# Kernel tuning notes

Measured on AMD Instinct MI355X. Metric: run time of the kernel, lower is better.

## Reference

```python
import jax, jax.numpy as jnp
import numpy as np

N = 50000      # nodes
E = 1600000    # message edges (avg degree 32)
EQ = 500000    # link-prediction query edges
IN, HID, OUT, FCH = 128, 128, 64, 256
ALPHA = 0.5


def setup_inputs() -> dict:
    key = jax.random.key(0)
    ks = jax.random.split(key, 8)
    def p(k, shape):
        fan_in = shape[0]
        return jax.random.normal(k, shape, jnp.float32) * (1.0 / np.sqrt(fan_in))
    return {
        "x": jax.random.normal(ks[0], (N, IN), jnp.float32),
        "edge_index": jax.random.randint(ks[1], (2, E), 0, N),
        "edge_label_index": jax.random.randint(ks[2], (2, EQ), 0, N),
        "W1": p(ks[3], (IN, HID)),  "b1": jnp.zeros((HID,), jnp.float32),
        "W2": p(ks[4], (HID, OUT)), "b2": jnp.zeros((OUT,), jnp.float32),
        "Wf1": p(ks[5], (IN, FCH)), "bf1": jnp.zeros((FCH,), jnp.float32),
        "Wf2": p(ks[6], (FCH, OUT)), "bf2": jnp.zeros((OUT,), jnp.float32),
    }


def reference(x, edge_index, edge_label_index, W1, b1, W2, b2, Wf1, bf1, Wf2, bf2):
    n = x.shape[0]
    # GCN self-loops + symmetric normalization (PyG GCNConv defaults)
    loop = jnp.arange(n)
    src = jnp.concatenate([edge_index[0], loop])
    dst = jnp.concatenate([edge_index[1], loop])
    deg = jax.ops.segment_sum(jnp.ones_like(dst, jnp.float32), dst, num_segments=n)
    dinv = jnp.where(deg > 0, jax.lax.rsqrt(deg), 0.0)
    norm = dinv[src] * dinv[dst]  # [E+N]

    def gcn(h, W, b):
        h = h @ W                                  # transform first (PyG order)
        msg = norm[:, None] * h[src]               # gather + scale per edge
        return jax.ops.segment_sum(msg, dst, num_segments=n) + b

    x_gcn = jax.nn.relu(gcn(x, W1, b1))
    x_gcn = gcn(x_gcn, W2, b2)
    x_fc = jax.nn.relu(x @ Wf1 + bf1) @ Wf2 + bf2
    z = x_gcn * (1.0 - ALPHA) + x_fc * ALPHA       # [N, OUT]
    # edge dot-product decode
    return jnp.sum(z[edge_label_index[0]] * z[edge_label_index[1]], axis=1)
```

## Files before the change

### kernel.cpp

```cpp
#include <hip/hip_runtime.h>

#define FIN   128
#define FHID  128
#define FOUT  64
#define FFC   256
#define CHUNK 8192
#define BKBITS 7
#define BKN   128
#define ECAP  4608

typedef __attribute__((ext_vector_type(8))) short          bf16x8;
typedef __attribute__((ext_vector_type(4))) float          f32x4;
typedef __attribute__((ext_vector_type(2))) float          f32x2;
typedef __attribute__((ext_vector_type(8))) unsigned short u16x8;

static __device__ __forceinline__ unsigned short f2bf(float f) {
    unsigned int u = __float_as_uint(f);
    u = (u + 0x7fffu + ((u >> 16) & 1u)) >> 16;
    return (unsigned short)u;
}
static __device__ __forceinline__ float bf2f(unsigned short s) {
    return __uint_as_float(((unsigned int)s) << 16);
}

__global__ __launch_bounds__(256) void cvt_binA_kernel(
    const float* __restrict__ x, const float* __restrict__ W1,
    const float* __restrict__ W2, const float* __restrict__ Wf1,
    const float* __restrict__ Wf2,
    unsigned short* __restrict__ xbf, unsigned short* __restrict__ w1t,
    unsigned short* __restrict__ w2t, unsigned short* __restrict__ wf1t,
    unsigned short* __restrict__ wf2t, long n4,
    const int* __restrict__ src, const int* __restrict__ dst,
    int* __restrict__ bcur, unsigned int* __restrict__ ebuf, int E, int NBA)
{
    int t = threadIdx.x;
    if (blockIdx.x < NBA) {
        __shared__ int hist[512];
        __shared__ int rstart[512];
        __shared__ int lcur[512];
        hist[t] = 0; hist[t + 256] = 0; lcur[t] = 0; lcur[t + 256] = 0;
        __syncthreads();
        int e0 = blockIdx.x * CHUNK;
        int e1 = min(e0 + CHUNK, E);
        for (int e = e0 + t; e < e1; e += 256)
            atomicAdd(&hist[dst[e] >> BKBITS], 1);
        __syncthreads();
        if (hist[t])       rstart[t]       = atomicAdd(&bcur[t],       hist[t]);
        if (hist[t + 256]) rstart[t + 256] = atomicAdd(&bcur[t + 256], hist[t + 256]);
        __syncthreads();
        for (int e = e0 + t; e < e1; e += 256) {
            int s = src[e], d = dst[e];
            int b = d >> BKBITS;
            int pos = rstart[b] + atomicAdd(&lcur[b], 1);
            if (pos < ECAP)
                ebuf[(size_t)b * ECAP + pos] =
                    ((unsigned)s << BKBITS) | ((unsigned)d & (BKN - 1));
        }
        return;
    }
    long i = (long)(blockIdx.x - NBA) * 256 + t;
    if (i < 16384) {
        int k = (int)i >> 7, n = (int)i & 127;
        w1t[n * 128 + k] = f2bf(W1[i]);
    } else if (i < 24576) {
        int j = (int)i - 16384; int k = j >> 6, n = j & 63;
        w2t[n * 128 + k] = f2bf(W2[j]);
    } else if (i < 57344) {
        int j = (int)i - 24576; int k = j >> 8, n = j & 255;
        wf1t[n * 128 + k] = f2bf(Wf1[j]);
    } else if (i < 73728) {
        int j = (int)i - 57344; int k = j >> 6, n = j & 63;
        wf2t[n * 256 + k] = f2bf(Wf2[j]);
    } else {
        long xt = i - 73728;
        long g = xt >> 8;
        int  tt = (int)(xt & 255);
        long b0 = g * 1024 + tt;
        #pragma unroll
        for (int k = 0; k < 4; k++) {
            long idx = b0 + (long)k * 256;
            if (idx < n4) {
                float4 v = ((const float4*)x)[idx];
                ushort4 o = make_ushort4(f2bf(v.x), f2bf(v.y), f2bf(v.z), f2bf(v.w));
                ((ushort4*)xbf)[idx] = o;
            }
        }
    }
}

__global__ __launch_bounds__(256) void binB_kernel(
    const unsigned int* __restrict__ ebuf, const int* __restrict__ bcnt,
    int2* __restrict__ rp2, int* __restrict__ col, float* __restrict__ dinv,
    const unsigned short* __restrict__ xbf, unsigned char* __restrict__ xs,
    int N)
{
    __shared__ int cnt[128];
    __shared__ int tmp[256];
    __shared__ int ccur[128];
    __shared__ int scur[256];
    __shared__ float sdinv[128];
    __shared__ unsigned int skey[ECAP];
    int b = blockIdx.x;
    int t = threadIdx.x;
    size_t base = (size_t)b * ECAP;
    int ne = min(bcnt[b], ECAP);
    if (t < 128) cnt[t] = 0;
    scur[t] = 0;
    __syncthreads();
    for (int e = t; e < ne; e += 256) {
        unsigned int k = ebuf[base + e];
        atomicAdd(&cnt[k & (BKN - 1)], 1);
        atomicAdd(&scur[k >> 15], 1);
    }
    __syncthreads();
    int c = (t < 128) ? cnt[t] : 0;
    tmp[t] = c;
    __syncthreads();
    int acc = c;
    for (int off = 1; off < 128; off <<= 1) {
        int a = (t >= off) ? tmp[t - off] : 0;
        __syncthreads();
        acc += a; tmp[t] = acc;
        __syncthreads();
    }
    if (t < 128) {
        float di = rsqrtf((float)c + 1.0f);
        sdinv[t] = di;
        int node = b * BKN + t;
        int st = (int)base + acc - c;
        if (node < N) { dinv[node] = di; rp2[node] = make_int2(st, st + c); }
        ccur[t] = st;
    }
    __syncthreads();
    int sv = scur[t];
    tmp[t] = sv;
    __syncthreads();
    int sacc = sv;
    for (int off = 1; off < 256; off <<= 1) {
        int a = (t >= off) ? tmp[t - off] : 0;
        __syncthreads();
        sacc += a; tmp[t] = sacc;
        __syncthreads();
    }
    scur[t] = sacc - sv;
    __syncthreads();
    for (int e = t; e < ne; e += 256) {
        unsigned int k = ebuf[base + e];
        int pos = atomicAdd(&scur[k >> 15], 1);
        skey[pos] = k;
    }
    __syncthreads();
    for (int w = 0; w < ne; w += 256) {
        int e = w + t;
        if (e < ne) {
            unsigned int k = skey[e];
            int pos = atomicAdd(&ccur[k & (BKN - 1)], 1);
            col[pos] = (int)(k >> BKBITS);
        }
        __syncthreads();
    }
    int nl0 = t >> 3;
    int f0 = (t & 7) << 4;
    #pragma unroll
    for (int it = 0; it < 4; it++) {
        int nl = it * 32 + nl0;
        int gn = b * BKN + nl;
        if (gn >= N) continue;
        float d2 = sdinv[nl];
        const unsigned short* xr = xbf + (size_t)gn * FIN + f0;
        u16x8 v0 = *(const u16x8*)xr;
        u16x8 v1 = *(const u16x8*)(xr + 8);
        float f[16];
        #pragma unroll
        for (int j = 0; j < 8; j++) {
            f[j]     = d2 * bf2f((unsigned short)v0[j]);
            f[8 + j] = d2 * bf2f((unsigned short)v1[j]);
        }
        uint4 w;
        w.x = 0; w.y = 0; w.z = 0; w.w = 0;
        w.x = __builtin_amdgcn_cvt_pk_fp8_f32(f[0],  f[1],  w.x, false);
        w.x = __builtin_amdgcn_cvt_pk_fp8_f32(f[2],  f[3],  w.x, true);
        w.y = __builtin_amdgcn_cvt_pk_fp8_f32(f[4],  f[5],  w.y, false);
        w.y = __builtin_amdgcn_cvt_pk_fp8_f32(f[6],  f[7],  w.y, true);
        w.z = __builtin_amdgcn_cvt_pk_fp8_f32(f[8],  f[9],  w.z, false);
        w.z = __builtin_amdgcn_cvt_pk_fp8_f32(f[10], f[11], w.z, true);
        w.w = __builtin_amdgcn_cvt_pk_fp8_f32(f[12], f[13], w.w, false);
        w.w = __builtin_amdgcn_cvt_pk_fp8_f32(f[14], f[15], w.w, true);
        *(uint4*)(xs + (size_t)gn * 128 + f0) = w;
    }
}

__global__ __launch_bounds__(256) void fc_fused_kernel(
    const unsigned short* __restrict__ A,
    const unsigned short* __restrict__ B1T,
    const unsigned short* __restrict__ B2T,
    const float* __restrict__ bias1, const float* __restrict__ bias2,
    float* __restrict__ C, int M)
{
    __shared__ __align__(16) unsigned short lds[32768];
    const int tid  = threadIdx.x;
    const int lane = tid & 63;
    const int wave = tid >> 6;
    const int m = lane & 15;
    const int q = lane >> 4;
    const int rowbase = blockIdx.x * 64 + wave * 16;
    const int row = rowbase + m;

    #pragma unroll 4
    for (int i = tid; i < 4096; i += 256) {
        int ck = i >> 4, sl = i & 15;
        ((u16x8*)lds)[(ck << 4) | (sl ^ (ck & 7))] = ((const u16x8*)B1T)[i];
    }
    __syncthreads();

    f32x4 acc[16] = {};
    const unsigned short* arow = A + (size_t)row * FIN + q * 8;
    for (int k0 = 0; k0 < 128; k0 += 32) {
        bf16x8 a = {};
        if (row < M) a = *(const bf16x8*)(arow + k0);
        int sl = q + (k0 >> 3);
        #pragma unroll
        for (int c = 0; c < 16; c++) {
            int cc = c * 16 + m;
            bf16x8 b = ((const bf16x8*)lds)[(cc << 4) | (sl ^ (cc & 7))];
            acc[c] = __builtin_amdgcn_mfma_f32_16x16x32_bf16(a, b, acc[c], 0, 0, 0);
        }
    }
    __syncthreads();

    #pragma unroll 2
    for (int i = tid; i < 2048; i += 256) {
        int ck = i >> 5, sl = i & 31;
        ((u16x8*)lds)[2048 + ((ck << 5) | (sl ^ (ck & 7)))] = ((const u16x8*)B2T)[i];
    }
    #pragma unroll
    for (int c = 0; c < 16; c++) {
        int cc = c * 16 + m;
        float bv = bias1[cc];
        #pragma unroll
        for (int r = 0; r < 4; r++) {
            int rr = wave * 16 + q * 4 + r;
            float v = fmaxf(acc[c][r] + bv, 0.f);
            lds[rr * 256 + ((((cc >> 3) ^ (rr & 7)) << 3) | (cc & 7))] = f2bf(v);
        }
    }
    __syncthreads();

    f32x4 acc2[4] = {};
    {
        int rr = wave * 16 + m;
        for (int k0 = 0; k0 < 256; k0 += 32) {
            int sl = q + (k0 >> 3);
            bf16x8 a = ((const bf16x8*)lds)[(rr << 5) | (sl ^ (rr & 7))];
            #pragma unroll
            for (int c = 0; c < 4; c++) {
                int cc = c * 16 + m;
                bf16x8 b = ((const bf16x8*)lds)[2048 + ((cc << 5) | (sl ^ (cc & 7)))];
                acc2[c] = __builtin_amdgcn_mfma_f32_16x16x32_bf16(a, b, acc2[c], 0, 0, 0);
            }
        }
    }
    __syncthreads();

    constexpr int ROWB = 4 * 16 * 4 + 16;
    unsigned char* wbase = (unsigned char*)lds + wave * 16 * ROWB;
    #pragma unroll
    for (int c = 0; c < 4; c++) {
        int lc = c * 16 + m;
        float bv = bias2[lc];
        #pragma unroll
        for (int r = 0; r < 4; r++)
            ((float*)(wbase + (q * 4 + r) * ROWB))[lc] = acc2[c][r] + bv;
    }
    #pragma unroll
    for (int p = 0; p < 4; p++) {
        int r2 = p * 4 + (lane >> 4);
        int bo = (lane & 15) * 16;
        int gr = rowbase + r2;
        if (gr < M) {
            uint4 v = *(const uint4*)(wbase + r2 * ROWB + bo);
            *(uint4*)((unsigned char*)C + (size_t)gr * FOUT * 4 + bo) = v;
        }
    }
}

__global__ __launch_bounds__(256) void gcn_fused_kernel(
    const unsigned short* __restrict__ A,
    const unsigned short* __restrict__ B1T,
    const unsigned short* __restrict__ B2T,
    const float* __restrict__ bias1,
    const float* __restrict__ rowscale,
    unsigned short* __restrict__ C, int M)
{
    __shared__ __align__(16) unsigned short lds[24576];
    const int tid  = threadIdx.x;
    const int lane = tid & 63;
    const int wave = tid >> 6;
    const int m = lane & 15;
    const int q = lane >> 4;
    const int rowbase = blockIdx.x * 64 + wave * 16;
    const int row = rowbase + m;

    #pragma unroll 2
    for (int i = tid; i < 2048; i += 256) {
        int ck = i >> 4, sl = i & 15;
        ((u16x8*)lds)[(ck << 4) | (sl ^ (ck & 7))] = ((const u16x8*)B1T)[i];
    }
    #pragma unroll 2
    for (int i = tid; i < 1024; i += 256) {
        int ck = i >> 4, sl = i & 15;
        ((u16x8*)lds)[2048 + ((ck << 4) | (sl ^ (ck & 7)))] = ((const u16x8*)B2T)[i];
    }
    __syncthreads();

    f32x4 acc[8] = {};
    const unsigned short* arow = A + (size_t)row * FIN + q * 8;
    for (int k0 = 0; k0 < 128; k0 += 32) {
        bf16x8 a = {};
        if (row < M) a = *(const bf16x8*)(arow + k0);
        int sl = q + (k0 >> 3);
        #pragma unroll
        for (int c = 0; c < 8; c++) {
            int cc = c * 16 + m;
            bf16x8 b = ((const bf16x8*)lds)[(cc << 4) | (sl ^ (cc & 7))];
            acc[c] = __builtin_amdgcn_mfma_f32_16x16x32_bf16(a, b, acc[c], 0, 0, 0);
        }
    }
    __syncthreads();

    #pragma unroll
    for (int c = 0; c < 8; c++) {
        int cc = c * 16 + m;
        float bv = bias1[cc];
        #pragma unroll
        for (int r = 0; r < 4; r++) {
            int rr = wave * 16 + q * 4 + r;
            float v = fmaxf(acc[c][r] + bv, 0.f);
            lds[rr * 128 + ((((cc >> 3) ^ (rr & 7)) << 3) | (cc & 7))] = f2bf(v);
        }
    }
    __syncthreads();

    f32x4 acc2[4] = {};
    {
        int rr = wave * 16 + m;
        for (int k0 = 0; k0 < 128; k0 += 32) {
            int sl = q + (k0 >> 3);
            bf16x8 a = ((const bf16x8*)lds)[(rr << 4) | (sl ^ (rr & 7))];
            #pragma unroll
            for (int c = 0; c < 4; c++) {
                int cc = c * 16 + m;
                bf16x8 b = ((const bf16x8*)lds)[2048 + ((cc << 4) | (sl ^ (cc & 7)))];
                acc2[c] = __builtin_amdgcn_mfma_f32_16x16x32_bf16(a, b, acc2[c], 0, 0, 0);
            }
        }
    }
    float rs[4];
    #pragma unroll
    for (int r = 0; r < 4; r++) {
        int gr = rowbase + q * 4 + r;
        rs[r] = (gr < M) ? rowscale[gr] : 1.0f;
    }
    __syncthreads();

    constexpr int ROWB = 4 * 16 * 2 + 16;
    unsigned char* wbase = (unsigned char*)lds + wave * 16 * ROWB;
    #pragma unroll
    for (int c = 0; c < 4; c++) {
        int lc = c * 16 + m;
        #pragma unroll
        for (int r = 0; r < 4; r++)
            ((unsigned short*)(wbase + (q * 4 + r) * ROWB))[lc] =
                f2bf(acc2[c][r] * rs[r]);
    }
    #pragma unroll
    for (int p = 0; p < 2; p++) {
        int r2 = p * 8 + (lane >> 3);
        int bo = (lane & 7) * 16;
        int gr = rowbase + r2;
        if (gr < M) {
            uint4 v = *(const uint4*)(wbase + r2 * ROWB + bo);
            *(uint4*)((unsigned char*)C + (size_t)gr * FOUT * 2 + bo) = v;
        }
    }
}

__global__ __launch_bounds__(256) void pull1_kernel(
    const unsigned char* __restrict__ xs, const int2* __restrict__ rp2,
    const int* __restrict__ col, const float* __restrict__ dinv,
    unsigned short* __restrict__ aggx, int N)
{
    int tid = threadIdx.x;
    int node = blockIdx.x * 32 + (tid >> 3);
    if (node >= N) return;
    int f0 = (tid & 7) << 4;
    const unsigned char* base = xs + f0;
    float acc[16] = {};
    auto accum = [&](uint4 g) {
        f32x2 p;
        p = __builtin_amdgcn_cvt_pk_f32_fp8(g.x, false); acc[0]  += p.x; acc[1]  += p.y;
        p = __builtin_amdgcn_cvt_pk_f32_fp8(g.x, true);  acc[2]  += p.x; acc[3]  += p.y;
        p = __builtin_amdgcn_cvt_pk_f32_fp8(g.y, false); acc[4]  += p.x; acc[5]  += p.y;
        p = __builtin_amdgcn_cvt_pk_f32_fp8(g.y, true);  acc[6]  += p.x; acc[7]  += p.y;
        p = __builtin_amdgcn_cvt_pk_f32_fp8(g.z, false); acc[8]  += p.x; acc[9]  += p.y;
        p = __builtin_amdgcn_cvt_pk_f32_fp8(g.z, true);  acc[10] += p.x; acc[11] += p.y;
        p = __builtin_amdgcn_cvt_pk_f32_fp8(g.w, false); acc[12] += p.x; acc[13] += p.y;
        p = __builtin_amdgcn_cvt_pk_f32_fp8(g.w, true);  acc[14] += p.x; acc[15] += p.y;
    };
    accum(*(const uint4*)(base + (size_t)node * 128));
    int2 se = rp2[node];
    int e = se.x, end = se.y;
    for (; e + 4 <= end; e += 4) {
        int s0 = col[e], s1 = col[e + 1], s2 = col[e + 2], s3 = col[e + 3];
        uint4 g0 = *(const uint4*)(base + (size_t)s0 * 128);
        uint4 g1 = *(const uint4*)(base + (size_t)s1 * 128);
        uint4 g2 = *(const uint4*)(base + (size_t)s2 * 128);
        uint4 g3 = *(const uint4*)(base + (size_t)s3 * 128);
        accum(g0); accum(g1); accum(g2); accum(g3);
    }
    for (; e < end; e++)
        accum(*(const uint4*)(base + (size_t)col[e] * 128));
    float di = dinv[node];
    u16x8 o0, o1;
    #pragma unroll
    for (int j = 0; j < 8; j++) {
        o0[j] = f2bf(di * acc[j]);
        o1[j] = f2bf(di * acc[8 + j]);
    }
    *(u16x8*)(aggx + (size_t)node * FIN + f0)     = o0;
    *(u16x8*)(aggx + (size_t)node * FIN + f0 + 8) = o1;
}

__global__ __launch_bounds__(256) void pull2_kernel(
    const unsigned short* __restrict__ t2s, const int2* __restrict__ rp2,
    const int* __restrict__ col, const float* __restrict__ dinv,
    const float* __restrict__ xfc, const float* __restrict__ b2,
    unsigned short* __restrict__ zbf, int N)
{
    int tid = threadIdx.x;
    int node = blockIdx.x * 32 + (tid >> 3);
    if (node >= N) return;
    int f0 = (tid & 7) << 3;
    const unsigned short* base = t2s + f0;
    u16x8 own = *(const u16x8*)(base + (size_t)node * FOUT);
    float acc[8];
    #pragma unroll
    for (int j = 0; j < 8; j++) acc[j] = bf2f(own[j]);
    int2 se = rp2[node];
    int e = se.x, end = se.y;
    for (; e + 4 <= end; e += 4) {
        int s0 = col[e], s1 = col[e + 1], s2 = col[e + 2], s3 = col[e + 3];
        u16x8 v0 = *(const u16x8*)(base + (size_t)s0 * FOUT);
        u16x8 v1 = *(const u16x8*)(base + (size_t)s1 * FOUT);
        u16x8 v2 = *(const u16x8*)(base + (size_t)s2 * FOUT);
        u16x8 v3 = *(const u16x8*)(base + (size_t)s3 * FOUT);
        #pragma unroll
        for (int j = 0; j < 8; j++)
            acc[j] += (bf2f(v0[j]) + bf2f(v1[j])) + (bf2f(v2[j]) + bf2f(v3[j]));
    }
    for (; e < end; e++) {
        u16x8 v = *(const u16x8*)(base + (size_t)col[e] * FOUT);
        #pragma unroll
        for (int j = 0; j < 8; j++) acc[j] += bf2f(v[j]);
    }
    float di = dinv[node];
    float4 x0 = *(const float4*)(xfc + (size_t)node * FOUT + f0);
    float4 x1 = *(const float4*)(xfc + (size_t)node * FOUT + f0 + 4);
    float4 bb0 = *(const float4*)(b2 + f0);
    float4 bb1 = *(const float4*)(b2 + f0 + 4);
    float xf[8] = { x0.x, x0.y, x0.z, x0.w, x1.x, x1.y, x1.z, x1.w };
    float bv[8] = { bb0.x, bb0.y, bb0.z, bb0.w, bb1.x, bb1.y, bb1.z, bb1.w };
    u16x8 o;
    #pragma unroll
    for (int j = 0; j < 8; j++)
        o[j] = f2bf(0.5f * (di * acc[j] + bv[j]) + 0.5f * xf[j]);
    *(u16x8*)(zbf + (size_t)node * FOUT + f0) = o;
}

__global__ void decode_kernel(
    const unsigned short* __restrict__ zbf, const int* __restrict__ eli,
    float* __restrict__ out, int Q)
{
    int tid = blockIdx.x * blockDim.x + threadIdx.x;
    int q = tid >> 3;
    if (q >= Q) return;
    int lane = tid & 7;
    int a = eli[q];
    int b = eli[Q + q];
    u16x8 va = *(const u16x8*)(zbf + (size_t)a * FOUT + lane * 8);
    u16x8 vb = *(const u16x8*)(zbf + (size_t)b * FOUT + lane * 8);
    float s = 0.f;
    #pragma unroll
    for (int j = 0; j < 8; j++) s += bf2f(va[j]) * bf2f(vb[j]);
    s += __shfl_down(s, 4, 8);
    s += __shfl_down(s, 2, 8);
    s += __shfl_down(s, 1, 8);
    if (lane == 0) out[q] = s;
}

extern "C" void kernel_launch(void* const* d_in, const int* in_sizes, int n_in,
                              void* d_out, int out_size, void* d_ws, size_t ws_size,
                              hipStream_t stream)
{
    const float* x   = (const float*)d_in[0];
    const int*   ei  = (const int*)  d_in[1];
    const int*   eli = (const int*)  d_in[2];
    const float* W1  = (const float*)d_in[3];
    const float* b1  = (const float*)d_in[4];
    const float* W2  = (const float*)d_in[5];
    const float* b2  = (const float*)d_in[6];
    const float* Wf1 = (const float*)d_in[7];
    const float* bf1 = (const float*)d_in[8];
    const float* Wf2 = (const float*)d_in[9];
    const float* bf2 = (const float*)d_in[10];
    float* out = (float*)d_out;

    const int N = in_sizes[0] / FIN;
    const int E = in_sizes[1] / 2;
    const int Q = in_sizes[2] / 2;
    const int* src = ei;
    const int* dst = ei + E;
    const int NBK = (N + BKN - 1) >> BKBITS;
    const int NBA = (E + CHUNK - 1) / CHUNK;

    char* p = (char*)d_ws;
    float* dinv = (float*)p;             p += (size_t)N * 4;
    int2*  rp2  = (int2*)p;              p += (size_t)N * 8;
    int*   bcur = (int*)p;               p += 2048;
    unsigned short* xbf  = (unsigned short*)p; p += (size_t)N * FIN * 2;
    unsigned short* w1t  = (unsigned short*)p; p += FIN * FHID * 2;
    unsigned short* w2t  = (unsigned short*)p; p += FHID * FOUT * 2;
    unsigned short* wf1t = (unsigned short*)p; p += FIN * FFC * 2;
    unsigned short* wf2t = (unsigned short*)p; p += FFC * FOUT * 2;
    float* xfc = (float*)p;              p += (size_t)N * FOUT * 4;
    unsigned char* xs = (unsigned char*)p;     p += (size_t)N * 128;
    unsigned int* ebuf = (unsigned int*)p;  p += (size_t)NBK * ECAP * 4;
    int*   col  = (int*)p;               p += (size_t)NBK * ECAP * 4;
    unsigned short* aggx = (unsigned short*)p; p += (size_t)N * FIN * 2;
    unsigned short* t2s  = (unsigned short*)p; p += (size_t)N * FOUT * 2;
    unsigned short* zbf  = (unsigned short*)p; p += (size_t)N * FOUT * 2;

    const int TB = 256;

    hipMemsetAsync(bcur, 0, 2048, stream);

    {
        long n4 = (long)N * FIN / 4;
        long xThreads = (n4 + 3) / 4;
        long cvtThreads = 73728 + xThreads;
        int cvtBlocks = (int)((cvtThreads + TB - 1) / TB);
        cvt_binA_kernel<<<NBA + cvtBlocks, TB, 0, stream>>>(
            x, W1, W2, Wf1, Wf2, xbf, w1t, w2t, wf1t, wf2t, n4,
            src, dst, bcur, ebuf, E, NBA);
    }

    fc_fused_kernel<<<(N + 63) / 64, TB, 0, stream>>>(
        xbf, wf1t, wf2t, bf1, bf2, xfc, N);

    binB_kernel<<<NBK, TB, 0, stream>>>(ebuf, bcur, rp2, col, dinv, xbf, xs, N);

    pull1_kernel<<<(N + 31) / 32, TB, 0, stream>>>(xs, rp2, col, dinv, aggx, N);

    gcn_fused_kernel<<<(N + 63) / 64, TB, 0, stream>>>(
        aggx, w1t, w2t, b1, dinv, t2s, N);

    pull2_kernel<<<(N + 31) / 32, TB, 0, stream>>>(
        t2s, rp2, col, dinv, xfc, b2, zbf, N);

    {
        long total = (long)Q * 8;
        decode_kernel<<<(int)((total + TB - 1) / TB), TB, 0, stream>>>(
            zbf, eli, out, Q);
    }
}
```

Baseline: 257.1 us.

## Fuse first-layer aggregation into GCN GEMM kernel and drop bf16 conversion pass

Removes the separate conversion kernel. x is now read as fp32 directly in the FC GEMM and in binB, and each GEMM block converts and transposes its weights to bf16 in LDS. The first-layer pull aggregation moves into gcn_fused_kernel, so aggregated rows go straight to LDS instead of round-tripping through a global aggx buffer. Binning becomes its own kernel with a smaller chunk, giving more blocks. The cost is that every GEMM block redoes the weight conversion with strided fp32 loads, fp32 x reads double the bytes, and the gather now shares a kernel with the MFMA work, which may lower occupancy.

```diff
diff --git a/kernel.cpp b/kernel.cpp
--- a/kernel.cpp
+++ b/kernel.cpp
@@ -4,7 +4,7 @@
 #define FHID  128
 #define FOUT  64
 #define FFC   256
-#define CHUNK 8192
+#define CHUNK 4096
 #define BKBITS 7
 #define BKN   128
 #define ECAP  4608
@@ -22,76 +22,50 @@
 static __device__ __forceinline__ float bf2f(unsigned short s) {
     return __uint_as_float(((unsigned int)s) << 16);
 }
-
-__global__ __launch_bounds__(256) void cvt_binA_kernel(
-    const float* __restrict__ x, const float* __restrict__ W1,
-    const float* __restrict__ W2, const float* __restrict__ Wf1,
-    const float* __restrict__ Wf2,
-    unsigned short* __restrict__ xbf, unsigned short* __restrict__ w1t,
-    unsigned short* __restrict__ w2t, unsigned short* __restrict__ wf1t,
-    unsigned short* __restrict__ wf2t, long n4,
+static __device__ __forceinline__ void accum_fp8(float* acc, uint4 g) {
+    f32x2 p;
+    p = __builtin_amdgcn_cvt_pk_f32_fp8(g.x, false); acc[0]  += p.x; acc[1]  += p.y;
+    p = __builtin_amdgcn_cvt_pk_f32_fp8(g.x, true);  acc[2]  += p.x; acc[3]  += p.y;
+    p = __builtin_amdgcn_cvt_pk_f32_fp8(g.y, false); acc[4]  += p.x; acc[5]  += p.y;
+    p = __builtin_amdgcn_cvt_pk_f32_fp8(g.y, true);  acc[6]  += p.x; acc[7]  += p.y;
+    p = __builtin_amdgcn_cvt_pk_f32_fp8(g.z, false); acc[8]  += p.x; acc[9]  += p.y;
+    p = __builtin_amdgcn_cvt_pk_f32_fp8(g.z, true);  acc[10] += p.x; acc[11] += p.y;
+    p = __builtin_amdgcn_cvt_pk_f32_fp8(g.w, false); acc[12] += p.x; acc[13] += p.y;
+    p = __builtin_amdgcn_cvt_pk_f32_fp8(g.w, true);  acc[14] += p.x; acc[15] += p.y;
+}
+
+__global__ __launch_bounds__(256) void binA_kernel(
     const int* __restrict__ src, const int* __restrict__ dst,
-    int* __restrict__ bcur, unsigned int* __restrict__ ebuf, int E, int NBA)
-{
+    int* __restrict__ bcur, unsigned int* __restrict__ ebuf, int E)
+{
+    __shared__ int hist[512];
+    __shared__ int rstart[512];
+    __shared__ int lcur[512];
     int t = threadIdx.x;
-    if (blockIdx.x < NBA) {
-        __shared__ int hist[512];
-        __shared__ int rstart[512];
-        __shared__ int lcur[512];
-        hist[t] = 0; hist[t + 256] = 0; lcur[t] = 0; lcur[t + 256] = 0;
-        __syncthreads();
-        int e0 = blockIdx.x * CHUNK;
-        int e1 = min(e0 + CHUNK, E);
-        for (int e = e0 + t; e < e1; e += 256)
-            atomicAdd(&hist[dst[e] >> BKBITS], 1);
-        __syncthreads();
-        if (hist[t])       rstart[t]       = atomicAdd(&bcur[t],       hist[t]);
-        if (hist[t + 256]) rstart[t + 256] = atomicAdd(&bcur[t + 256], hist[t + 256]);
-        __syncthreads();
-        for (int e = e0 + t; e < e1; e += 256) {
-            int s = src[e], d = dst[e];
-            int b = d >> BKBITS;
-            int pos = rstart[b] + atomicAdd(&lcur[b], 1);
-            if (pos < ECAP)
-                ebuf[(size_t)b * ECAP + pos] =
-                    ((unsigned)s << BKBITS) | ((unsigned)d & (BKN - 1));
-        }
-        return;
-    }
-    long i = (long)(blockIdx.x - NBA) * 256 + t;
-    if (i < 16384) {
-        int k = (int)i >> 7, n = (int)i & 127;
-        w1t[n * 128 + k] = f2bf(W1[i]);
-    } else if (i < 24576) {
-        int j = (int)i - 16384; int k = j >> 6, n = j & 63;
-        w2t[n * 128 + k] = f2bf(W2[j]);
-    } else if (i < 57344) {
-        int j = (int)i - 24576; int k = j >> 8, n = j & 255;
-        wf1t[n * 128 + k] = f2bf(Wf1[j]);
-    } else if (i < 73728) {
-        int j = (int)i - 57344; int k = j >> 6, n = j & 63;
-        wf2t[n * 256 + k] = f2bf(Wf2[j]);
-    } else {
-        long xt = i - 73728;
-        long g = xt >> 8;
-        int  tt = (int)(xt & 255);
-        long b0 = g * 1024 + tt;
-        #pragma unroll
-        for (int k = 0; k < 4; k++) {
-            long idx = b0 + (long)k * 256;
-            if (idx < n4) {
-                float4 v = ((const float4*)x)[idx];
-                ushort4 o = make_ushort4(f2bf(v.x), f2bf(v.y), f2bf(v.z), f2bf(v.w));
-                ((ushort4*)xbf)[idx] = o;
-            }
-        }
+    hist[t] = 0; hist[t + 256] = 0; lcur[t] = 0; lcur[t + 256] = 0;
+    __syncthreads();
+    int e0 = blockIdx.x * CHUNK;
+    int e1 = min(e0 + CHUNK, E);
+    for (int e = e0 + t; e < e1; e += 256)
+        atomicAdd(&hist[dst[e] >> BKBITS], 1);
+    __syncthreads();
+    if (hist[t])       rstart[t]       = atomicAdd(&bcur[t],       hist[t]);
+    if (hist[t + 256]) rstart[t + 256] = atomicAdd(&bcur[t + 256], hist[t + 256]);
+    __syncthreads();
+    for (int e = e0 + t; e < e1; e += 256) {
+        int s = src[e], d = dst[e];
+        int b = d >> BKBITS;
+        int pos = rstart[b] + atomicAdd(&lcur[b], 1);
+        if (pos < ECAP)
+            ebuf[(size_t)b * ECAP + pos] =
+                ((unsigned)s << BKBITS) | ((unsigned)d & (BKN - 1));
     }
 }
 
 __global__ __launch_bounds__(256) void binB_kernel(
     const unsigned int* __restrict__ ebuf, const int* __restrict__ bcnt,
     int2* __restrict__ rp2, int* __restrict__ col, float* __restrict__ dinv,
-    const unsigned short* __restrict__ xbf, unsigned char* __restrict__ xs,
+    const float* __restrict__ x, unsigned char* __restrict__ xs,
     int N)
 {
     __shared__ int cnt[128];
@@ -167,15 +141,15 @@
         int gn = b * BKN + nl;
         if (gn >= N) continue;
         float d2 = sdinv[nl];
-        const unsigned short* xr = xbf + (size_t)gn * FIN + f0;
-        u16x8 v0 = *(const u16x8*)xr;
-        u16x8 v1 = *(const u16x8*)(xr + 8);
-        float f[16];
-        #pragma unroll
-        for (int j = 0; j < 8; j++) {
-            f[j]     = d2 * bf2f((unsigned short)v0[j]);
-            f[8 + j] = d2 * bf2f((unsigned short)v1[j]);
-        }
+        const float* xr = x + (size_t)gn * FIN + f0;
+        float4 va = *(const float4*)(xr);
+        float4 vb = *(const float4*)(xr + 4);
+        float4 vc = *(const float4*)(xr + 8);
+        float4 vd = *(const float4*)(xr + 12);
+        float f[16] = { va.x * d2, va.y * d2, va.z * d2, va.w * d2,
+                        vb.x * d2, vb.y * d2, vb.z * d2, vb.w * d2,
+                        vc.x * d2, vc.y * d2, vc.z * d2, vc.w * d2,
+                        vd.x * d2, vd.y * d2, vd.z * d2, vd.w * d2 };
         uint4 w;
         w.x = 0; w.y = 0; w.z = 0; w.w = 0;
         w.x = __builtin_amdgcn_cvt_pk_fp8_f32(f[0],  f[1],  w.x, false);
@@ -191,9 +165,9 @@
 }
 
 __global__ __launch_bounds__(256) void fc_fused_kernel(
-    const unsigned short* __restrict__ A,
-    const unsigned short* __restrict__ B1T,
-    const unsigned short* __restrict__ B2T,
+    const float* __restrict__ X,
+    const float* __restrict__ Wf1,
+    const float* __restrict__ Wf2,
     const float* __restrict__ bias1, const float* __restrict__ bias2,
     float* __restrict__ C, int M)
 {
@@ -206,18 +180,27 @@
     const int rowbase = blockIdx.x * 64 + wave * 16;
     const int row = rowbase + m;
 
-    #pragma unroll 4
     for (int i = tid; i < 4096; i += 256) {
-        int ck = i >> 4, sl = i & 15;
-        ((u16x8*)lds)[(ck << 4) | (sl ^ (ck & 7))] = ((const u16x8*)B1T)[i];
+        int sl = i >> 8, n = i & 255;
+        u16x8 o;
+        #pragma unroll
+        for (int j = 0; j < 8; j++) o[j] = f2bf(Wf1[(sl * 8 + j) * 256 + n]);
+        ((u16x8*)lds)[(n << 4) | (sl ^ (n & 7))] = o;
     }
     __syncthreads();
 
     f32x4 acc[16] = {};
-    const unsigned short* arow = A + (size_t)row * FIN + q * 8;
+    const float* arow = X + (size_t)row * FIN + q * 8;
     for (int k0 = 0; k0 < 128; k0 += 32) {
         bf16x8 a = {};
-        if (row < M) a = *(const bf16x8*)(arow + k0);
+        if (row < M) {
+            float4 a0 = *(const float4*)(arow + k0);
+            float4 a1 = *(const float4*)(arow + k0 + 4);
+            a[0] = (short)f2bf(a0.x); a[1] = (short)f2bf(a0.y);
+            a[2] = (short)f2bf(a0.z); a[3] = (short)f2bf(a0.w);
+            a[4] = (short)f2bf(a1.x); a[5] = (short)f2bf(a1.y);
+            a[6] = (short)f2bf(a1.z); a[7] = (short)f2bf(a1.w);
+        }
         int sl = q + (k0 >> 3);
         #pragma unroll
         for (int c = 0; c < 16; c++) {
@@ -228,10 +211,12 @@
     }
     __syncthreads();
 
-    #pragma unroll 2
     for (int i = tid; i < 2048; i += 256) {
-        int ck = i >> 5, sl = i & 31;
-        ((u16x8*)lds)[2048 + ((ck << 5) | (sl ^ (ck & 7)))] = ((const u16x8*)B2T)[i];
+        int sl = i >> 6, n = i & 63;
+        u16x8 o;
+        #pragma unroll
+        for (int j = 0; j < 8; j++) o[j] = f2bf(Wf2[(sl * 8 + j) * 64 + n]);
+        ((u16x8*)lds)[2048 + ((n << 5) | (sl ^ (n & 7)))] = o;
     }
     #pragma unroll
     for (int c = 0; c < 16; c++) {
@@ -285,44 +270,85 @@
 }
 
 __global__ __launch_bounds__(256) void gcn_fused_kernel(
-    const unsigned short* __restrict__ A,
-    const unsigned short* __restrict__ B1T,
-    const unsigned short* __restrict__ B2T,
+    const unsigned char* __restrict__ xs, const int2* __restrict__ rp2,
+    const int* __restrict__ col, const float* __restrict__ dinv,
+    const float* __restrict__ W1,
+    const float* __restrict__ W2,
     const float* __restrict__ bias1,
-    const float* __restrict__ rowscale,
     unsigned short* __restrict__ C, int M)
 {
-    __shared__ __align__(16) unsigned short lds[24576];
+    __shared__ __align__(16) unsigned short lds[32768];
     const int tid  = threadIdx.x;
     const int lane = tid & 63;
     const int wave = tid >> 6;
     const int m = lane & 15;
     const int q = lane >> 4;
     const int rowbase = blockIdx.x * 64 + wave * 16;
-    const int row = rowbase + m;
-
-    #pragma unroll 2
+
     for (int i = tid; i < 2048; i += 256) {
-        int ck = i >> 4, sl = i & 15;
-        ((u16x8*)lds)[(ck << 4) | (sl ^ (ck & 7))] = ((const u16x8*)B1T)[i];
-    }
-    #pragma unroll 2
+        int sl = i >> 7, n = i & 127;
+        u16x8 o;
+        #pragma unroll
+        for (int j = 0; j < 8; j++) o[j] = f2bf(W1[(sl * 8 + j) * 128 + n]);
+        ((u16x8*)lds)[1024 + ((n << 4) | (sl ^ (n & 7)))] = o;
+    }
     for (int i = tid; i < 1024; i += 256) {
-        int ck = i >> 4, sl = i & 15;
-        ((u16x8*)lds)[2048 + ((ck << 4) | (sl ^ (ck & 7)))] = ((const u16x8*)B2T)[i];
+        int sl = i >> 6, n = i & 63;
+        u16x8 o;
+        #pragma unroll
+        for (int j = 0; j < 8; j++) o[j] = f2bf(W2[(sl * 8 + j) * 64 + n]);
+        ((u16x8*)lds)[3072 + ((n << 4) | (sl ^ (n & 7)))] = o;
+    }
+
+    {
+        int nls = tid >> 3;
+        int f0 = (tid & 7) << 4;
+        int c80 = (tid & 7) * 2;
+        const unsigned char* gbase = xs + f0;
+        #pragma unroll
+        for (int pass = 0; pass < 2; pass++) {
+            int lnl = pass * 32 + nls;
+            int node = blockIdx.x * 64 + lnl;
+            u16x8 o0 = {}, o1 = {};
+            if (node < M) {
+                float acc[16] = {};
+                accum_fp8(acc, *(const uint4*)(gbase + (size_t)node * 128));
+                int2 se = rp2[node];
+                int e = se.x, end = se.y;
+                for (; e + 4 <= end; e += 4) {
+                    int s0 = col[e], s1 = col[e + 1];
+                    int s2 = col[e + 2], s3 = col[e + 3];
+                    uint4 g0 = *(const uint4*)(gbase + (size_t)s0 * 128);
+                    uint4 g1 = *(const uint4*)(gbase + (size_t)s1 * 128);
+                    uint4 g2 = *(const uint4*)(gbase + (size_t)s2 * 128);
+                    uint4 g3 = *(const uint4*)(gbase + (size_t)s3 * 128);
+                    accum_fp8(acc, g0); accum_fp8(acc, g1);
+                    accum_fp8(acc, g2); accum_fp8(acc, g3);
+                }
+                for (; e < end; e++)
+                    accum_fp8(acc, *(const uint4*)(gbase + (size_t)col[e] * 128));
+                float di = dinv[node];
+                #pragma unroll
+                for (int j = 0; j < 8; j++) {
+                    o0[j] = f2bf(di * acc[j]);
+                    o1[j] = f2bf(di * acc[8 + j]);
+                }
+            }
+            ((u16x8*)lds)[lnl * 16 + (c80 ^ (lnl & 7))]       = o0;
+            ((u16x8*)lds)[lnl * 16 + ((c80 + 1) ^ (lnl & 7))] = o1;
+        }
     }
     __syncthreads();
 
     f32x4 acc[8] = {};
-    const unsigned short* arow = A + (size_t)row * FIN + q * 8;
     for (int k0 = 0; k0 < 128; k0 += 32) {
-        bf16x8 a = {};
-        if (row < M) a = *(const bf16x8*)(arow + k0);
         int sl = q + (k0 >> 3);
+        int lr = wave * 16 + m;
+        bf16x8 a = ((const bf16x8*)lds)[lr * 16 + (sl ^ (lr & 7))];
         #pragma unroll
         for (int c = 0; c < 8; c++) {
             int cc = c * 16 + m;
-            bf16x8 b = ((const bf16x8*)lds)[(cc << 4) | (sl ^ (cc & 7))];
+            bf16x8 b = ((const bf16x8*)lds)[1024 + ((cc << 4) | (sl ^ (cc & 7)))];
             acc[c] = __builtin_amdgcn_mfma_f32_16x16x32_bf16(a, b, acc[c], 0, 0, 0);
         }
     }
@@ -336,7 +362,7 @@
         for (int r = 0; r < 4; r++) {
             int rr = wave * 16 + q * 4 + r;
             float v = fmaxf(acc[c][r] + bv, 0.f);
-            lds[rr * 128 + ((((cc >> 3) ^ (rr & 7)) << 3) | (cc & 7))] = f2bf(v);
+            lds[8192 + rr * 128 + ((((cc >> 3) ^ (rr & 7)) << 3) | (cc & 7))] = f2bf(v);
         }
     }
     __syncthreads();
@@ -346,11 +372,11 @@
         int rr = wave * 16 + m;
         for (int k0 = 0; k0 < 128; k0 += 32) {
             int sl = q + (k0 >> 3);
-            bf16x8 a = ((const bf16x8*)lds)[(rr << 4) | (sl ^ (rr & 7))];
+            bf16x8 a = ((const bf16x8*)lds)[1024 + ((rr << 4) | (sl ^ (rr & 7)))];
             #pragma unroll
             for (int c = 0; c < 4; c++) {
                 int cc = c * 16 + m;
-                bf16x8 b = ((const bf16x8*)lds)[2048 + ((cc << 4) | (sl ^ (cc & 7)))];
+                bf16x8 b = ((const bf16x8*)lds)[3072 + ((cc << 4) | (sl ^ (cc & 7)))];
                 acc2[c] = __builtin_amdgcn_mfma_f32_16x16x32_bf16(a, b, acc2[c], 0, 0, 0);
             }
         }
@@ -359,7 +385,7 @@
     #pragma unroll
     for (int r = 0; r < 4; r++) {
         int gr = rowbase + q * 4 + r;
-        rs[r] = (gr < M) ? rowscale[gr] : 1.0f;
+        rs[r] = (gr < M) ? dinv[gr] : 1.0f;
     }
     __syncthreads();
 
@@ -383,52 +409,6 @@
             *(uint4*)((unsigned char*)C + (size_t)gr * FOUT * 2 + bo) = v;
         }
     }
-}
-
-__global__ __launch_bounds__(256) void pull1_kernel(
-    const unsigned char* __restrict__ xs, const int2* __restrict__ rp2,
-    const int* __restrict__ col, const float* __restrict__ dinv,
-    unsigned short* __restrict__ aggx, int N)
-{
-    int tid = threadIdx.x;
-    int node = blockIdx.x * 32 + (tid >> 3);
-    if (node >= N) return;
-    int f0 = (tid & 7) << 4;
-    const unsigned char* base = xs + f0;
-    float acc[16] = {};
-    auto accum = [&](uint4 g) {
-        f32x2 p;
-        p = __builtin_amdgcn_cvt_pk_f32_fp8(g.x, false); acc[0]  += p.x; acc[1]  += p.y;
-        p = __builtin_amdgcn_cvt_pk_f32_fp8(g.x, true);  acc[2]  += p.x; acc[3]  += p.y;
-        p = __builtin_amdgcn_cvt_pk_f32_fp8(g.y, false); acc[4]  += p.x; acc[5]  += p.y;
-        p = __builtin_amdgcn_cvt_pk_f32_fp8(g.y, true);  acc[6]  += p.x; acc[7]  += p.y;
-        p = __builtin_amdgcn_cvt_pk_f32_fp8(g.z, false); acc[8]  += p.x; acc[9]  += p.y;
-        p = __builtin_amdgcn_cvt_pk_f32_fp8(g.z, true);  acc[10] += p.x; acc[11] += p.y;
-        p = __builtin_amdgcn_cvt_pk_f32_fp8(g.w, false); acc[12] += p.x; acc[13] += p.y;
-        p = __builtin_amdgcn_cvt_pk_f32_fp8(g.w, true);  acc[14] += p.x; acc[15] += p.y;
-    };
-    accum(*(const uint4*)(base + (size_t)node * 128));
-    int2 se = rp2[node];
-    int e = se.x, end = se.y;
-    for (; e + 4 <= end; e += 4) {
-        int s0 = col[e], s1 = col[e + 1], s2 = col[e + 2], s3 = col[e + 3];
-        uint4 g0 = *(const uint4*)(base + (size_t)s0 * 128);
-        uint4 g1 = *(const uint4*)(base + (size_t)s1 * 128);
-        uint4 g2 = *(const uint4*)(base + (size_t)s2 * 128);
-        uint4 g3 = *(const uint4*)(base + (size_t)s3 * 128);
-        accum(g0); accum(g1); accum(g2); accum(g3);
-    }
-    for (; e < end; e++)
-        accum(*(const uint4*)(base + (size_t)col[e] * 128));
-    float di = dinv[node];
-    u16x8 o0, o1;
-    #pragma unroll
-    for (int j = 0; j < 8; j++) {
-        o0[j] = f2bf(di * acc[j]);
-        o1[j] = f2bf(di * acc[8 + j]);
-    }
-    *(u16x8*)(aggx + (size_t)node * FIN + f0)     = o0;
-    *(u16x8*)(aggx + (size_t)node * FIN + f0 + 8) = o1;
 }
 
 __global__ __launch_bounds__(256) void pull2_kernel(
@@ -527,16 +507,10 @@
     float* dinv = (float*)p;             p += (size_t)N * 4;
     int2*  rp2  = (int2*)p;              p += (size_t)N * 8;
     int*   bcur = (int*)p;               p += 2048;
-    unsigned short* xbf  = (unsigned short*)p; p += (size_t)N * FIN * 2;
-    unsigned short* w1t  = (unsigned short*)p; p += FIN * FHID * 2;
-    unsigned short* w2t  = (unsigned short*)p; p += FHID * FOUT * 2;
-    unsigned short* wf1t = (unsigned short*)p; p += FIN * FFC * 2;
-    unsigned short* wf2t = (unsigned short*)p; p += FFC * FOUT * 2;
     float* xfc = (float*)p;              p += (size_t)N * FOUT * 4;
     unsigned char* xs = (unsigned char*)p;     p += (size_t)N * 128;
     unsigned int* ebuf = (unsigned int*)p;  p += (size_t)NBK * ECAP * 4;
     int*   col  = (int*)p;               p += (size_t)NBK * ECAP * 4;
-    unsigned short* aggx = (unsigned short*)p; p += (size_t)N * FIN * 2;
     unsigned short* t2s  = (unsigned short*)p; p += (size_t)N * FOUT * 2;
     unsigned short* zbf  = (unsigned short*)p; p += (size_t)N * FOUT * 2;
 
@@ -544,25 +518,15 @@
 
     hipMemsetAsync(bcur, 0, 2048, stream);
 
-    {
-        long n4 = (long)N * FIN / 4;
-        long xThreads = (n4 + 3) / 4;
-        long cvtThreads = 73728 + xThreads;
-        int cvtBlocks = (int)((cvtThreads + TB - 1) / TB);
-        cvt_binA_kernel<<<NBA + cvtBlocks, TB, 0, stream>>>(
-            x, W1, W2, Wf1, Wf2, xbf, w1t, w2t, wf1t, wf2t, n4,
-            src, dst, bcur, ebuf, E, NBA);
-    }
-
     fc_fused_kernel<<<(N + 63) / 64, TB, 0, stream>>>(
-        xbf, wf1t, wf2t, bf1, bf2, xfc, N);
-
-    binB_kernel<<<NBK, TB, 0, stream>>>(ebuf, bcur, rp2, col, dinv, xbf, xs, N);
-
-    pull1_kernel<<<(N + 31) / 32, TB, 0, stream>>>(xs, rp2, col, dinv, aggx, N);
+        x, Wf1, Wf2, bf1, bf2, xfc, N);
+
+    binA_kernel<<<NBA, TB, 0, stream>>>(src, dst, bcur, ebuf, E);
+
+    binB_kernel<<<NBK, TB, 0, stream>>>(ebuf, bcur, rp2, col, dinv, x, xs, N);
 
     gcn_fused_kernel<<<(N + 63) / 64, TB, 0, stream>>>(
-        aggx, w1t, w2t, b1, dinv, t2s, N);
+        xs, rp2, col, dinv, W1, W2, b1, t2s, N);
 
     pull2_kernel<<<(N + 31) / 32, TB, 0, stream>>>(
         t2s, rp2, col, dinv, xfc, b2, zbf, N);
```

Result: slower. 272.5 us (+6.0%).
